# Kernel optimization log

Measured on AMD Instinct MI355X. Metric: run time of the kernel, lower is better.

Reference implementation:

```python
import jax, jax.numpy as jnp
import numpy as np

FEATURE_DIM = 128
NUM_EDGES = 640000
NUM_NODES = 40000


def setup_inputs() -> dict:
    key = jax.random.key(0)
    ks = jax.random.split(key, 10)
    d = FEATURE_DIM
    scale = 1.0 / np.sqrt(d)
    inp = {
        "messages": jax.random.normal(ks[0], (NUM_EDGES, d), dtype=jnp.float32),
        "receivers": jax.random.randint(ks[1], (NUM_EDGES,), 0, NUM_NODES, dtype=jnp.int32),
        "num_segments": NUM_NODES,
        "Wk": jax.random.normal(ks[2], (d, d), dtype=jnp.float32) * scale,
        "bk": jnp.zeros((d,), dtype=jnp.float32),
        "Wv": jax.random.normal(ks[3], (d, d), dtype=jnp.float32) * scale,
        "bv": jnp.zeros((d,), dtype=jnp.float32),
        "Wq": jax.random.normal(ks[4], (d, d), dtype=jnp.float32) * scale,
        "bq": jnp.zeros((d,), dtype=jnp.float32),
        "Wo": jax.random.normal(ks[5], (d, d), dtype=jnp.float32) * scale,
        "bo": jnp.zeros((d,), dtype=jnp.float32),
    }
    return inp


def reference(messages, receivers, num_segments, Wk, bk, Wv, bv, Wq, bq, Wo, bo):
    d = messages.shape[-1]
    # per-edge key/value projections
    keys = messages @ Wk + bk            # [E, d]
    values = messages @ Wv + bv          # [E, d]
    # node-level summed messages -> queries
    summed = jax.ops.segment_sum(messages, receivers, num_segments)  # [N, d]
    queries = summed @ Wq + bq                                       # [N, d]
    # scalar attention score per edge (dot over full feature dim)
    msg_q = queries[receivers]                                       # [E, d]
    scores = jnp.sum(msg_q * keys, axis=-1) / jnp.sqrt(jnp.float32(d))  # [E]
    # segment softmax over edges sharing a receiver
    max_s = jax.ops.segment_max(scores, receivers, num_segments)     # [N]
    exp_s = jnp.exp(scores - max_s[receivers])                       # [E]
    sum_e = jax.ops.segment_sum(exp_s, receivers, num_segments)      # [N]
    attn = exp_s / (sum_e[receivers] + 1e-08)                        # [E]
    # weighted scatter-sum of values, then output projection
    agg = jax.ops.segment_sum(values * attn[:, None], receivers, num_segments)  # [N, d]
    return agg @ Wo + bo
```

## Files before the change

### kernel.cpp

```cpp
#include <hip/hip_runtime.h>

#define D 128
#define RSQRT_D 0.088388347648318440550f
#define NEG_HUGE -3.4e38f
#define NPB 8
#define CAP 288
#define DTHR 20.0f

#define FMA4(acc, s, b) { acc.x += (s)*(b).x; acc.y += (s)*(b).y; acc.z += (s)*(b).z; acc.w += (s)*(b).w; }
#define ADD4(acc, b) { acc.x += (b).x; acc.y += (b).y; acc.z += (b).z; acc.w += (b).w; }
#define MRG4(a) { a.x += __shfl_xor(a.x,32); a.y += __shfl_xor(a.y,32); a.z += __shfl_xor(a.z,32); a.w += __shfl_xor(a.w,32); }
#define SCL4(a, f) { a.x *= (f); a.y *= (f); a.z *= (f); a.w *= (f); }
#define Z4 make_float4(0.f,0.f,0.f,0.f)

#define MERGE_HALVES(mi, si, ci) { \
    float mo_ = __shfl_xor(mi, 32); \
    float so_ = __shfl_xor(si, 32); \
    float4 co_; co_.x = __shfl_xor(ci.x, 32); co_.y = __shfl_xor(ci.y, 32); \
    co_.z = __shfl_xor(ci.z, 32); co_.w = __shfl_xor(ci.w, 32); \
    float mt_ = fmaxf(mi, mo_); \
    float e0_ = __expf(mi - mt_), e1_ = __expf(mo_ - mt_); \
    si = si * e0_ + so_ * e1_; \
    ci.x = ci.x * e0_ + co_.x * e1_; ci.y = ci.y * e0_ + co_.y * e1_; \
    ci.z = ci.z * e0_ + co_.z * e1_; ci.w = ci.w * e0_ + co_.w * e1_; \
}

__global__ __launch_bounds__(256) void prep_kernel(
    const float* __restrict__ Wq, const float* __restrict__ Wk,
    const float* __restrict__ bq, const float* __restrict__ bk,
    const float* __restrict__ Wv, const float* __restrict__ Wo,
    const float* __restrict__ bv,
    float* __restrict__ Wqk, float* __restrict__ bqk,
    float* __restrict__ wqb, float* __restrict__ bqb,
    float* __restrict__ Wvo, float* __restrict__ bvo,
    int* __restrict__ zbase, int zcount) {
    int bid = blockIdx.x, t = threadIdx.x;
    if (bid < 64) {
        int i = bid * 2 + (t >> 7), j = t & 127;
        float a1 = 0.f, a2 = 0.f;
        for (int u = 0; u < D; ++u) {
            a1 += Wq[i * D + u] * Wk[j * D + u];
            a2 += Wv[i * D + u] * Wo[u * D + j];
        }
        Wqk[i * D + j] = a1;
        Wvo[i * D + j] = a2;
    } else if (bid == 64) {
        if (t < D) {
            int j = t;
            float a1 = 0.f, a2 = 0.f, a3 = 0.f;
            for (int u = 0; u < D; ++u) {
                a1 += bq[u] * Wk[j * D + u];
                a2 += Wq[j * D + u] * bk[u];
                a3 += bv[u] * Wo[u * D + j];
            }
            bqk[j] = a1; wqb[j] = a2; bvo[j] = a3;
            if (j == 0) {
                float b = 0.f;
                for (int u = 0; u < D; ++u) b += bq[u] * bk[u];
                *bqb = b;
            }
        }
    } else {
        int idx = (bid - 65) * 256 + t;
        if (idx < zcount) zbase[idx] = 0;
    }
}

__global__ void hist_kernel(const int* __restrict__ recv, int* __restrict__ cnt, int E) {
    int i = blockIdx.x * blockDim.x + threadIdx.x;
    int base = i << 2;
    if (base + 3 < E) {
        int4 r = *(const int4*)(recv + base);
        atomicAdd(&cnt[r.x], 1);
        atomicAdd(&cnt[r.y], 1);
        atomicAdd(&cnt[r.z], 1);
        atomicAdd(&cnt[r.w], 1);
    } else {
        for (int u = base; u < E; ++u) atomicAdd(&cnt[recv[u]], 1);
    }
}

__global__ __launch_bounds__(1024) void scan_kernel(const int* __restrict__ cnt,
                                                    int* __restrict__ start, int N) {
    __shared__ int wsum[16];
    __shared__ int chunk_total;
    int t = threadIdx.x;
    int w = t >> 6, lane = t & 63;
    int running = 0;
    const int4* cnt4 = (const int4*)cnt;
    int nIter = (N + 4095) >> 12;
    int4 v = make_int4(0, 0, 0, 0);
    {
        int i = t << 2;
        if (i < N) v = cnt4[i >> 2];
    }
    for (int it = 0; it < nIter; ++it) {
        int4 vn = make_int4(0, 0, 0, 0);
        {
            int i = ((it + 1) << 12) + (t << 2);
            if (it + 1 < nIter && i < N) vn = cnt4[i >> 2];
        }
        int s0 = v.x, s1 = s0 + v.y, s2 = s1 + v.z, s3 = s2 + v.w;
        int x = s3;
#pragma unroll
        for (int off = 1; off < 64; off <<= 1) {
            int y = __shfl_up(x, off);
            if (lane >= off) x += y;
        }
        if (lane == 63) wsum[w] = x;
        __syncthreads();
        if (w == 0 && lane < 16) {
            int s = wsum[lane];
#pragma unroll
            for (int off = 1; off < 16; off <<= 1) {
                int y = __shfl_up(s, off);
                if (lane >= off) s += y;
            }
            wsum[lane] = s;
            if (lane == 15) chunk_total = s;
        }
        __syncthreads();
        int waveoff = (w == 0) ? 0 : wsum[w - 1];
        int tb = running + waveoff + (x - s3);
        int i = (it << 12) + (t << 2);
        if (i < N) ((int4*)start)[i >> 2] = make_int4(tb, tb + s0, tb + s1, tb + s2);
        running += chunk_total;
        __syncthreads();
        v = vn;
    }
    if (t == 0) start[N] = running;
}

__global__ void fill_kernel(const int* __restrict__ recv, const int* __restrict__ start,
                            int* __restrict__ cursor, int* __restrict__ eidx, int E) {
    int e = blockIdx.x * blockDim.x + threadIdx.x;
    if (e >= E) return;
    int r = recv[e];
    int p = atomicAdd(&cursor[r], 1);
    eidx[start[r] + p] = e;
}

__device__ __forceinline__ float hdot32(float4 f, float4 q) {
    float p = f.x * q.x + f.y * q.y + f.z * q.z + f.w * q.w;
    p += __shfl_xor(p, 1); p += __shfl_xor(p, 2); p += __shfl_xor(p, 4);
    p += __shfl_xor(p, 8); p += __shfl_xor(p, 16);
    return p;
}

#define P1STEP(u, Fx) { \
    int r = j + h + 2 * (u); \
    float4 g_ = Fx; \
    float mk_ = (r < b4) ? 1.f : 0.f; \
    g_.x *= mk_; g_.y *= mk_; g_.z *= mk_; g_.w *= mk_; \
    if (r < b1)      { ADD4(a0, g_); } \
    else if (r < b2) { ADD4(a1, g_); } \
    else if (r < b3) { ADD4(a2, g_); } \
    else             { ADD4(a3, g_); } \
}

#define P3STEP(u, Fx) { \
    int r = j + h + 2 * (u); \
    bool valid_ = r < b4; \
    float4 f_ = Fx; \
    float4 qv_ = (r < b1) ? q0 : (r < b2) ? q1 : (r < b3) ? q2 : q3; \
    float qbv_ = (r < b1) ? qb0 : (r < b2) ? qb1 : (r < b3) ? qb2 : qb3; \
    float sc_ = (hdot32(f_, qv_) + qbv_) * RSQRT_D; \
    float msel_ = (r < b1) ? m0 : (r < b2) ? m1 : (r < b3) ? m2 : m3; \
    if (valid_ && sc_ > msel_ + DTHR) { \
        float fac_ = __expf(msel_ - sc_); \
        if (r < b1)      { sm0 *= fac_; SCL4(c0, fac_); m0 = sc_; } \
        else if (r < b2) { sm1 *= fac_; SCL4(c1, fac_); m1 = sc_; } \
        else if (r < b3) { sm2 *= fac_; SCL4(c2, fac_); m2 = sc_; } \
        else             { sm3 *= fac_; SCL4(c3, fac_); m3 = sc_; } \
        msel_ = sc_; \
    } \
    float wgt_ = valid_ ? __expf(sc_ - msel_) : 0.f; \
    if (r < b1)      { sm0 += wgt_; FMA4(c0, wgt_, f_); } \
    else if (r < b2) { sm1 += wgt_; FMA4(c1, wgt_, f_); } \
    else if (r < b3) { sm2 += wgt_; FMA4(c2, wgt_, f_); } \
    else             { sm3 += wgt_; FMA4(c3, wgt_, f_); } \
}

__global__ __launch_bounds__(128, 3) void mega_kernel(
    const float* __restrict__ msg, const int* __restrict__ eidx,
    const int* __restrict__ start,
    const float* __restrict__ Wqk, const float* __restrict__ bqk,
    const float* __restrict__ wqb, const float* __restrict__ bqbp,
    const float* __restrict__ Wvo, const float* __restrict__ bvo,
    const float* __restrict__ bo,
    float* __restrict__ out, int N) {
    __shared__ float4 sums4[NPB * 32];
    __shared__ float4 qks4[NPB * 32];
    __shared__ int eidx_s[CAP];
    __shared__ float sat[NPB];

    int t = threadIdx.x;
    int lane = t & 63, w = t >> 6;
    int h = lane >> 5;
    int k = lane & 31;
    int base = blockIdx.x * NPB;
    const float4* msg4 = (const float4*)msg;

    int nendB = min(base + NPB, N);
    int s0B = start[base];
    int cntB = start[nendB] - s0B;
    int cc = min(cntB, CAP);
    for (int i = t; i < cc; i += 128) eidx_s[i] = eidx[s0B + i];

    int n0 = base + w * 4;
    int b0 = start[min(n0 + 0, N)] - s0B;
    int b1 = start[min(n0 + 1, N)] - s0B;
    int b2 = start[min(n0 + 2, N)] - s0B;
    int b3 = start[min(n0 + 3, N)] - s0B;
    int b4 = start[min(n0 + 4, N)] - s0B;

    __syncthreads();

    auto loadrow = [&](int r) -> float4 {
        int rI = min(r, b4 - 1);
        int e = (rI < CAP) ? eidx_s[rI] : eidx[s0B + rI];
        return msg4[(size_t)e * 32 + k];
    };

    float4 a0 = Z4, a1 = Z4, a2 = Z4, a3 = Z4;
    if (b0 < b4) {
        int j = b0;
        float4 F0 = loadrow(j + h),      F1 = loadrow(j + h + 2),
               F2 = loadrow(j + h + 4),  F3 = loadrow(j + h + 6),
               F4 = loadrow(j + h + 8),  F5 = loadrow(j + h + 10),
               F6 = loadrow(j + h + 12), F7 = loadrow(j + h + 14);
        for (;;) {
            int jn = j + 16;
            bool more = jn < b4;
            float4 G0, G1, G2, G3, G4, G5, G6, G7;
            if (more) {
                G0 = loadrow(jn + h);      G1 = loadrow(jn + h + 2);
                G2 = loadrow(jn + h + 4);  G3 = loadrow(jn + h + 6);
                G4 = loadrow(jn + h + 8);  G5 = loadrow(jn + h + 10);
                G6 = loadrow(jn + h + 12); G7 = loadrow(jn + h + 14);
            }
            P1STEP(0, F0); P1STEP(1, F1); P1STEP(2, F2); P1STEP(3, F3);
            P1STEP(4, F4); P1STEP(5, F5); P1STEP(6, F6); P1STEP(7, F7);
            if (!more) break;
            F0 = G0; F1 = G1; F2 = G2; F3 = G3;
            F4 = G4; F5 = G5; F6 = G6; F7 = G7;
            j = jn;
        }
    }
    MRG4(a0); MRG4(a1); MRG4(a2); MRG4(a3);
    if (lane < 32) {
        sums4[(w * 4 + 0) * 32 + k] = a0;
        sums4[(w * 4 + 1) * 32 + k] = a1;
        sums4[(w * 4 + 2) * 32 + k] = a2;
        sums4[(w * 4 + 3) * 32 + k] = a3;
    }
    __syncthreads();

    {
        int c = t & 31, slot = t >> 5;
        const float4* B4 = (const float4*)Wqk;
        float4 acc0 = ((const float4*)bqk)[c];
        float4 acc1 = acc0;
        for (int i = 0; i < D; i += 4) {
            float4 aA = sums4[slot * 32 + (i >> 2)];
            float4 aB = sums4[(slot + 4) * 32 + (i >> 2)];
            float4 c0 = B4[(i + 0) * 32 + c];
            float4 c1 = B4[(i + 1) * 32 + c];
            float4 c2 = B4[(i + 2) * 32 + c];
            float4 c3 = B4[(i + 3) * 32 + c];
            FMA4(acc0, aA.x, c0); FMA4(acc0, aA.y, c1); FMA4(acc0, aA.z, c2); FMA4(acc0, aA.w, c3);
            FMA4(acc1, aB.x, c0); FMA4(acc1, aB.y, c1); FMA4(acc1, aB.z, c2); FMA4(acc1, aB.w, c3);
        }
        qks4[slot * 32 + c] = acc0;
        qks4[(slot + 4) * 32 + c] = acc1;
    }
    __syncthreads();

    {
        float4 wv = ((const float4*)wqb)[k];
        float bqb = bqbp[0];
        float4 sv0 = sums4[(w * 4 + 0) * 32 + k];
        float4 sv1 = sums4[(w * 4 + 1) * 32 + k];
        float4 sv2 = sums4[(w * 4 + 2) * 32 + k];
        float4 sv3 = sums4[(w * 4 + 3) * 32 + k];
        float qb0 = hdot32(sv0, wv) + bqb;
        float qb1 = hdot32(sv1, wv) + bqb;
        float qb2 = hdot32(sv2, wv) + bqb;
        float qb3 = hdot32(sv3, wv) + bqb;
        float4 q0 = qks4[(w * 4 + 0) * 32 + k];
        float4 q1 = qks4[(w * 4 + 1) * 32 + k];
        float4 q2 = qks4[(w * 4 + 2) * 32 + k];
        float4 q3 = qks4[(w * 4 + 3) * 32 + k];

        float m0 = NEG_HUGE, m1 = NEG_HUGE, m2 = NEG_HUGE, m3 = NEG_HUGE;
        float sm0 = 0.f, sm1 = 0.f, sm2 = 0.f, sm3 = 0.f;
        float4 c0 = Z4, c1 = Z4, c2 = Z4, c3 = Z4;
        if (b0 < b4) {
            int j = b0;
            float4 F0 = loadrow(j + h),      F1 = loadrow(j + h + 2),
                   F2 = loadrow(j + h + 4),  F3 = loadrow(j + h + 6),
                   F4 = loadrow(j + h + 8),  F5 = loadrow(j + h + 10),
                   F6 = loadrow(j + h + 12), F7 = loadrow(j + h + 14);
            for (;;) {
                int jn = j + 16;
                bool more = jn < b4;
                float4 G0, G1, G2, G3, G4, G5, G6, G7;
                if (more) {
                    G0 = loadrow(jn + h);      G1 = loadrow(jn + h + 2);
                    G2 = loadrow(jn + h + 4);  G3 = loadrow(jn + h + 6);
                    G4 = loadrow(jn + h + 8);  G5 = loadrow(jn + h + 10);
                    G6 = loadrow(jn + h + 12); G7 = loadrow(jn + h + 14);
                }
                P3STEP(0, F0); P3STEP(1, F1); P3STEP(2, F2); P3STEP(3, F3);
                P3STEP(4, F4); P3STEP(5, F5); P3STEP(6, F6); P3STEP(7, F7);
                if (!more) break;
                F0 = G0; F1 = G1; F2 = G2; F3 = G3;
                F4 = G4; F5 = G5; F6 = G6; F7 = G7;
                j = jn;
            }
        }
        MERGE_HALVES(m0, sm0, c0);
        MERGE_HALVES(m1, sm1, c1);
        MERGE_HALVES(m2, sm2, c2);
        MERGE_HALVES(m3, sm3, c3);
        float inv0 = 1.f / (sm0 + 1e-8f);
        float inv1 = 1.f / (sm1 + 1e-8f);
        float inv2 = 1.f / (sm2 + 1e-8f);
        float inv3 = 1.f / (sm3 + 1e-8f);
        if (lane < 32) {
            sums4[(w * 4 + 0) * 32 + k] = make_float4(c0.x * inv0, c0.y * inv0, c0.z * inv0, c0.w * inv0);
            sums4[(w * 4 + 1) * 32 + k] = make_float4(c1.x * inv1, c1.y * inv1, c1.z * inv1, c1.w * inv1);
            sums4[(w * 4 + 2) * 32 + k] = make_float4(c2.x * inv2, c2.y * inv2, c2.z * inv2, c2.w * inv2);
            sums4[(w * 4 + 3) * 32 + k] = make_float4(c3.x * inv3, c3.y * inv3, c3.z * inv3, c3.w * inv3);
        }
        if (lane == 0) {
            sat[w * 4 + 0] = sm0 * inv0;
            sat[w * 4 + 1] = sm1 * inv1;
            sat[w * 4 + 2] = sm2 * inv2;
            sat[w * 4 + 3] = sm3 * inv3;
        }
    }
    __syncthreads();

    {
        int c = t & 31, slot = t >> 5;
        const float4* B4 = (const float4*)Wvo;
        float4 bo4 = ((const float4*)bo)[c];
        float4 bv4 = ((const float4*)bvo)[c];
        float sa0 = sat[slot], sa1 = sat[slot + 4];
        float4 acc0 = make_float4(bo4.x + sa0 * bv4.x, bo4.y + sa0 * bv4.y,
                                  bo4.z + sa0 * bv4.z, bo4.w + sa0 * bv4.w);
        float4 acc1 = make_float4(bo4.x + sa1 * bv4.x, bo4.y + sa1 * bv4.y,
                                  bo4.z + sa1 * bv4.z, bo4.w + sa1 * bv4.w);
        for (int i = 0; i < D; i += 4) {
            float4 aA = sums4[slot * 32 + (i >> 2)];
            float4 aB = sums4[(slot + 4) * 32 + (i >> 2)];
            float4 d0 = B4[(i + 0) * 32 + c];
            float4 d1 = B4[(i + 1) * 32 + c];
            float4 d2 = B4[(i + 2) * 32 + c];
            float4 d3 = B4[(i + 3) * 32 + c];
            FMA4(acc0, aA.x, d0); FMA4(acc0, aA.y, d1); FMA4(acc0, aA.z, d2); FMA4(acc0, aA.w, d3);
            FMA4(acc1, aB.x, d0); FMA4(acc1, aB.y, d1); FMA4(acc1, aB.z, d2); FMA4(acc1, aB.w, d3);
        }
        int nA = base + slot, nB = base + slot + 4;
        if (nA < N) ((float4*)(out + (size_t)nA * D))[c] = acc0;
        if (nB < N) ((float4*)(out + (size_t)nB * D))[c] = acc1;
    }
}


extern "C" void kernel_launch(void* const* d_in, const int* in_sizes, int n_in,
                              void* d_out, int out_size, void* d_ws, size_t ws_size,
                              hipStream_t stream) {
    const float* msg = (const float*)d_in[0];
    const int* recv = (const int*)d_in[1];
    const float* Wk = (const float*)d_in[3];
    const float* bk = (const float*)d_in[4];
    const float* Wv = (const float*)d_in[5];
    const float* bv = (const float*)d_in[6];
    const float* Wq = (const float*)d_in[7];
    const float* bq = (const float*)d_in[8];
    const float* Wo = (const float*)d_in[9];
    const float* bo = (const float*)d_in[10];
    float* out = (float*)d_out;

    int E = in_sizes[0] / D;
    int N = out_size / D;

    char* wsb = (char*)d_ws;
    size_t o = 0;
    auto alloc = [&](size_t elems) {
        void* p = wsb + o;
        o += (elems * 4 + 63) & ~(size_t)63;
        return p;
    };

    int* cnt    = (int*)alloc(2 * (size_t)N);
    int* cursor = cnt + N;
    int* start  = (int*)alloc(N + 1);
    int* eidx   = (int*)alloc(E);
    float* Wqk  = (float*)alloc(D * D);
    float* bqk  = (float*)alloc(D);
    float* wqb  = (float*)alloc(D);
    float* bqb  = (float*)alloc(1);
    float* Wvo  = (float*)alloc(D * D);
    float* bvo  = (float*)alloc(D);

    int zcount = 2 * N;
    int zblocks = (zcount + 255) / 256;
    prep_kernel<<<65 + zblocks, 256, 0, stream>>>(Wq, Wk, bq, bk, Wv, Wo, bv,
                                                  Wqk, bqk, wqb, bqb, Wvo, bvo,
                                                  cnt, zcount);
    int E4 = (E + 3) / 4;
    int nbE4 = (E4 + 255) / 256;
    hist_kernel<<<nbE4, 256, 0, stream>>>(recv, cnt, E);
    scan_kernel<<<1, 1024, 0, stream>>>(cnt, start, N);
    int nbE = (E + 255) / 256;
    fill_kernel<<<nbE, 256, 0, stream>>>(recv, start, cursor, eidx, E);
    mega_kernel<<<(N + NPB - 1) / NPB, 128, 0, stream>>>(msg, eidx, start, Wqk, bqk, wqb, bqb,
                                                         Wvo, bvo, bo, out, N);
}
```

Before: 708.8 us.

## Write gathered message rows to a receiver-sorted buffer for contiguous second pass

During the first segment-sum pass, each gathered message row is also written to a workspace buffer ordered by receiver. The second, softmax-weighted pass then reads that buffer contiguously instead of gathering through the edge index again. This replaces a random gather with a streaming write plus a streaming read, which adds about one extra full-size write and read of the messages. The prefetch depth is halved from 16 to 8 rows and the occupancy hint is raised from 3 to 4 blocks, presumably to cut register pressure. The path only runs when the workspace can hold E*D floats.

```diff
diff --git a/kernel.cpp b/kernel.cpp
--- a/kernel.cpp
+++ b/kernel.cpp
@@ -150,6 +150,7 @@
 #define P1STEP(u, Fx) { \
     int r = j + h + 2 * (u); \
     float4 g_ = Fx; \
+    if (PERM && r < b4) perm4w[(size_t)(s0B + r) * 32 + k] = g_; \
     float mk_ = (r < b4) ? 1.f : 0.f; \
     g_.x *= mk_; g_.y *= mk_; g_.z *= mk_; g_.w *= mk_; \
     if (r < b1)      { ADD4(a0, g_); } \
@@ -181,9 +182,10 @@
     else             { sm3 += wgt_; FMA4(c3, wgt_, f_); } \
 }
 
-__global__ __launch_bounds__(128, 3) void mega_kernel(
+template<int PERM>
+__global__ __launch_bounds__(128, 4) void mega_kernel(
     const float* __restrict__ msg, const int* __restrict__ eidx,
-    const int* __restrict__ start,
+    const int* __restrict__ start, float* __restrict__ perm,
     const float* __restrict__ Wqk, const float* __restrict__ bqk,
     const float* __restrict__ wqb, const float* __restrict__ bqbp,
     const float* __restrict__ Wvo, const float* __restrict__ bvo,
@@ -200,6 +202,8 @@
     int k = lane & 31;
     int base = blockIdx.x * NPB;
     const float4* msg4 = (const float4*)msg;
+    float4* perm4w = (float4*)perm;
+    const float4* perm4c = (const float4*)perm;
 
     int nendB = min(base + NPB, N);
     int s0B = start[base];
@@ -221,29 +225,28 @@
         int e = (rI < CAP) ? eidx_s[rI] : eidx[s0B + rI];
         return msg4[(size_t)e * 32 + k];
     };
+    auto loadrowP = [&](int r) -> float4 {
+        int rI = min(r, b4 - 1);
+        if (PERM) return perm4c[(size_t)(s0B + rI) * 32 + k];
+        else      return loadrow(rI);
+    };
 
     float4 a0 = Z4, a1 = Z4, a2 = Z4, a3 = Z4;
     if (b0 < b4) {
         int j = b0;
-        float4 F0 = loadrow(j + h),      F1 = loadrow(j + h + 2),
-               F2 = loadrow(j + h + 4),  F3 = loadrow(j + h + 6),
-               F4 = loadrow(j + h + 8),  F5 = loadrow(j + h + 10),
-               F6 = loadrow(j + h + 12), F7 = loadrow(j + h + 14);
+        float4 F0 = loadrow(j + h), F1 = loadrow(j + h + 2),
+               F2 = loadrow(j + h + 4), F3 = loadrow(j + h + 6);
         for (;;) {
-            int jn = j + 16;
+            int jn = j + 8;
             bool more = jn < b4;
-            float4 G0, G1, G2, G3, G4, G5, G6, G7;
+            float4 G0, G1, G2, G3;
             if (more) {
-                G0 = loadrow(jn + h);      G1 = loadrow(jn + h + 2);
-                G2 = loadrow(jn + h + 4);  G3 = loadrow(jn + h + 6);
-                G4 = loadrow(jn + h + 8);  G5 = loadrow(jn + h + 10);
-                G6 = loadrow(jn + h + 12); G7 = loadrow(jn + h + 14);
+                G0 = loadrow(jn + h); G1 = loadrow(jn + h + 2);
+                G2 = loadrow(jn + h + 4); G3 = loadrow(jn + h + 6);
             }
             P1STEP(0, F0); P1STEP(1, F1); P1STEP(2, F2); P1STEP(3, F3);
-            P1STEP(4, F4); P1STEP(5, F5); P1STEP(6, F6); P1STEP(7, F7);
             if (!more) break;
             F0 = G0; F1 = G1; F2 = G2; F3 = G3;
-            F4 = G4; F5 = G5; F6 = G6; F7 = G7;
             j = jn;
         }
     }
@@ -297,25 +300,19 @@
         float4 c0 = Z4, c1 = Z4, c2 = Z4, c3 = Z4;
         if (b0 < b4) {
             int j = b0;
-            float4 F0 = loadrow(j + h),      F1 = loadrow(j + h + 2),
-                   F2 = loadrow(j + h + 4),  F3 = loadrow(j + h + 6),
-                   F4 = loadrow(j + h + 8),  F5 = loadrow(j + h + 10),
-                   F6 = loadrow(j + h + 12), F7 = loadrow(j + h + 14);
+            float4 F0 = loadrowP(j + h), F1 = loadrowP(j + h + 2),
+                   F2 = loadrowP(j + h + 4), F3 = loadrowP(j + h + 6);
             for (;;) {
-                int jn = j + 16;
+                int jn = j + 8;
                 bool more = jn < b4;
-                float4 G0, G1, G2, G3, G4, G5, G6, G7;
+                float4 G0, G1, G2, G3;
                 if (more) {
-                    G0 = loadrow(jn + h);      G1 = loadrow(jn + h + 2);
-                    G2 = loadrow(jn + h + 4);  G3 = loadrow(jn + h + 6);
-                    G4 = loadrow(jn + h + 8);  G5 = loadrow(jn + h + 10);
-                    G6 = loadrow(jn + h + 12); G7 = loadrow(jn + h + 14);
+                    G0 = loadrowP(jn + h); G1 = loadrowP(jn + h + 2);
+                    G2 = loadrowP(jn + h + 4); G3 = loadrowP(jn + h + 6);
                 }
                 P3STEP(0, F0); P3STEP(1, F1); P3STEP(2, F2); P3STEP(3, F3);
-                P3STEP(4, F4); P3STEP(5, F5); P3STEP(6, F6); P3STEP(7, F7);
                 if (!more) break;
                 F0 = G0; F1 = G1; F2 = G2; F3 = G3;
-                F4 = G4; F5 = G5; F6 = G6; F7 = G7;
                 j = jn;
             }
         }
@@ -405,6 +402,8 @@
     float* bqb  = (float*)alloc(1);
     float* Wvo  = (float*)alloc(D * D);
     float* bvo  = (float*)alloc(D);
+    float* perm = (float*)(wsb + o);
+    bool use_perm = (o + (size_t)E * D * 4) <= ws_size;
 
     int zcount = 2 * N;
     int zblocks = (zcount + 255) / 256;
@@ -417,6 +416,12 @@
     scan_kernel<<<1, 1024, 0, stream>>>(cnt, start, N);
     int nbE = (E + 255) / 256;
     fill_kernel<<<nbE, 256, 0, stream>>>(recv, start, cursor, eidx, E);
-    mega_kernel<<<(N + NPB - 1) / NPB, 128, 0, stream>>>(msg, eidx, start, Wqk, bqk, wqb, bqb,
-                                                         Wvo, bvo, bo, out, N);
-}
+    int nblk = (N + NPB - 1) / NPB;
+    if (use_perm) {
+        mega_kernel<1><<<nblk, 128, 0, stream>>>(msg, eidx, start, perm, Wqk, bqk, wqb, bqb,
+                                                 Wvo, bvo, bo, out, N);
+    } else {
+        mega_kernel<0><<<nblk, 128, 0, stream>>>(msg, eidx, start, nullptr, Wqk, bqk, wqb, bqb,
+                                                 Wvo, bvo, bo, out, N);
+    }
+}
```

Result: no change. 712.5 us (+0.5%).

## Keep first 48 edge rows in registers across both passes to avoid reloading

Applied to the files above, without the earlier changes.

The first 48 gathered message rows of each warp's node group (about 6 per node at an average degree of 16 per node... per 4 nodes) are loaded once into 24 float4 registers and reused in both the segment-sum pass and the attention pass. Remaining edges fall back to a smaller 4-row software-pipelined loop. This aims to cut the second gather of message rows from memory, at the cost of much higher register pressure, which under launch_bounds(128,3) may cause spills or lower occupancy. The tail loop also has less memory-level parallelism than the previous 16-row prefetch.

```diff
diff --git a/kernel.cpp b/kernel.cpp
--- a/kernel.cpp
+++ b/kernel.cpp
@@ -181,6 +181,9 @@
     else             { sm3 += wgt_; FMA4(c3, wgt_, f_); } \
 }
 
+#define P1G(jo, Ra, Rb, Rc, Rd) { int j = b0 + (jo); P1STEP(0, Ra); P1STEP(1, Rb); P1STEP(2, Rc); P1STEP(3, Rd); }
+#define P3G(jo, Ra, Rb, Rc, Rd) { int j = b0 + (jo); P3STEP(0, Ra); P3STEP(1, Rb); P3STEP(2, Rc); P3STEP(3, Rd); }
+
 __global__ __launch_bounds__(128, 3) void mega_kernel(
     const float* __restrict__ msg, const int* __restrict__ eidx,
     const int* __restrict__ start,
@@ -222,29 +225,39 @@
         return msg4[(size_t)e * 32 + k];
     };
 
+    float4 R00 = Z4, R01 = Z4, R02 = Z4, R03 = Z4,
+           R10 = Z4, R11 = Z4, R12 = Z4, R13 = Z4,
+           R20 = Z4, R21 = Z4, R22 = Z4, R23 = Z4,
+           R30 = Z4, R31 = Z4, R32 = Z4, R33 = Z4,
+           R40 = Z4, R41 = Z4, R42 = Z4, R43 = Z4,
+           R50 = Z4, R51 = Z4, R52 = Z4, R53 = Z4;
+
     float4 a0 = Z4, a1 = Z4, a2 = Z4, a3 = Z4;
     if (b0 < b4) {
-        int j = b0;
-        float4 F0 = loadrow(j + h),      F1 = loadrow(j + h + 2),
-               F2 = loadrow(j + h + 4),  F3 = loadrow(j + h + 6),
-               F4 = loadrow(j + h + 8),  F5 = loadrow(j + h + 10),
-               F6 = loadrow(j + h + 12), F7 = loadrow(j + h + 14);
-        for (;;) {
-            int jn = j + 16;
-            bool more = jn < b4;
-            float4 G0, G1, G2, G3, G4, G5, G6, G7;
-            if (more) {
-                G0 = loadrow(jn + h);      G1 = loadrow(jn + h + 2);
-                G2 = loadrow(jn + h + 4);  G3 = loadrow(jn + h + 6);
-                G4 = loadrow(jn + h + 8);  G5 = loadrow(jn + h + 10);
-                G6 = loadrow(jn + h + 12); G7 = loadrow(jn + h + 14);
+        R00 = loadrow(b0 + h +  0); R01 = loadrow(b0 + h +  2); R02 = loadrow(b0 + h +  4); R03 = loadrow(b0 + h +  6);
+        R10 = loadrow(b0 + h +  8); R11 = loadrow(b0 + h + 10); R12 = loadrow(b0 + h + 12); R13 = loadrow(b0 + h + 14);
+        R20 = loadrow(b0 + h + 16); R21 = loadrow(b0 + h + 18); R22 = loadrow(b0 + h + 20); R23 = loadrow(b0 + h + 22);
+        R30 = loadrow(b0 + h + 24); R31 = loadrow(b0 + h + 26); R32 = loadrow(b0 + h + 28); R33 = loadrow(b0 + h + 30);
+        R40 = loadrow(b0 + h + 32); R41 = loadrow(b0 + h + 34); R42 = loadrow(b0 + h + 36); R43 = loadrow(b0 + h + 38);
+        R50 = loadrow(b0 + h + 40); R51 = loadrow(b0 + h + 42); R52 = loadrow(b0 + h + 44); R53 = loadrow(b0 + h + 46);
+        P1G( 0, R00, R01, R02, R03);
+        P1G( 8, R10, R11, R12, R13);
+        P1G(16, R20, R21, R22, R23);
+        P1G(24, R30, R31, R32, R33);
+        P1G(32, R40, R41, R42, R43);
+        P1G(40, R50, R51, R52, R53);
+        int j = b0 + 48;
+        if (j < b4) {
+            float4 F0 = loadrow(j + h), F1 = loadrow(j + h + 2);
+            for (;;) {
+                int jn = j + 4;
+                bool more = jn < b4;
+                float4 G0, G1;
+                if (more) { G0 = loadrow(jn + h); G1 = loadrow(jn + h + 2); }
+                P1STEP(0, F0); P1STEP(1, F1);
+                if (!more) break;
+                F0 = G0; F1 = G1; j = jn;
             }
-            P1STEP(0, F0); P1STEP(1, F1); P1STEP(2, F2); P1STEP(3, F3);
-            P1STEP(4, F4); P1STEP(5, F5); P1STEP(6, F6); P1STEP(7, F7);
-            if (!more) break;
-            F0 = G0; F1 = G1; F2 = G2; F3 = G3;
-            F4 = G4; F5 = G5; F6 = G6; F7 = G7;
-            j = jn;
         }
     }
     MRG4(a0); MRG4(a1); MRG4(a2); MRG4(a3);
@@ -264,12 +277,12 @@
         for (int i = 0; i < D; i += 4) {
             float4 aA = sums4[slot * 32 + (i >> 2)];
             float4 aB = sums4[(slot + 4) * 32 + (i >> 2)];
-            float4 c0 = B4[(i + 0) * 32 + c];
-            float4 c1 = B4[(i + 1) * 32 + c];
-            float4 c2 = B4[(i + 2) * 32 + c];
-            float4 c3 = B4[(i + 3) * 32 + c];
-            FMA4(acc0, aA.x, c0); FMA4(acc0, aA.y, c1); FMA4(acc0, aA.z, c2); FMA4(acc0, aA.w, c3);
-            FMA4(acc1, aB.x, c0); FMA4(acc1, aB.y, c1); FMA4(acc1, aB.z, c2); FMA4(acc1, aB.w, c3);
+            float4 w0 = B4[(i + 0) * 32 + c];
+            float4 w1 = B4[(i + 1) * 32 + c];
+            float4 w2 = B4[(i + 2) * 32 + c];
+            float4 w3 = B4[(i + 3) * 32 + c];
+            FMA4(acc0, aA.x, w0); FMA4(acc0, aA.y, w1); FMA4(acc0, aA.z, w2); FMA4(acc0, aA.w, w3);
+            FMA4(acc1, aB.x, w0); FMA4(acc1, aB.y, w1); FMA4(acc1, aB.z, w2); FMA4(acc1, aB.w, w3);
         }
         qks4[slot * 32 + c] = acc0;
         qks4[(slot + 4) * 32 + c] = acc1;
@@ -296,27 +309,24 @@
         float sm0 = 0.f, sm1 = 0.f, sm2 = 0.f, sm3 = 0.f;
         float4 c0 = Z4, c1 = Z4, c2 = Z4, c3 = Z4;
         if (b0 < b4) {
-            int j = b0;
-            float4 F0 = loadrow(j + h),      F1 = loadrow(j + h + 2),
-                   F2 = loadrow(j + h + 4),  F3 = loadrow(j + h + 6),
-                   F4 = loadrow(j + h + 8),  F5 = loadrow(j + h + 10),
-                   F6 = loadrow(j + h + 12), F7 = loadrow(j + h + 14);
-            for (;;) {
-                int jn = j + 16;
-                bool more = jn < b4;
-                float4 G0, G1, G2, G3, G4, G5, G6, G7;
-                if (more) {
-                    G0 = loadrow(jn + h);      G1 = loadrow(jn + h + 2);
-                    G2 = loadrow(jn + h + 4);  G3 = loadrow(jn + h + 6);
-                    G4 = loadrow(jn + h + 8);  G5 = loadrow(jn + h + 10);
-                    G6 = loadrow(jn + h + 12); G7 = loadrow(jn + h + 14);
+            P3G( 0, R00, R01, R02, R03);
+            P3G( 8, R10, R11, R12, R13);
+            P3G(16, R20, R21, R22, R23);
+            P3G(24, R30, R31, R32, R33);
+            P3G(32, R40, R41, R42, R43);
+            P3G(40, R50, R51, R52, R53);
+            int j = b0 + 48;
+            if (j < b4) {
+                float4 F0 = loadrow(j + h), F1 = loadrow(j + h + 2);
+                for (;;) {
+                    int jn = j + 4;
+                    bool more = jn < b4;
+                    float4 G0, G1;
+                    if (more) { G0 = loadrow(jn + h); G1 = loadrow(jn + h + 2); }
+                    P3STEP(0, F0); P3STEP(1, F1);
+                    if (!more) break;
+                    F0 = G0; F1 = G1; j = jn;
                 }
-                P3STEP(0, F0); P3STEP(1, F1); P3STEP(2, F2); P3STEP(3, F3);
-                P3STEP(4, F4); P3STEP(5, F5); P3STEP(6, F6); P3STEP(7, F7);
-                if (!more) break;
-                F0 = G0; F1 = G1; F2 = G2; F3 = G3;
-                F4 = G4; F5 = G5; F6 = G6; F7 = G7;
-                j = jn;
             }
         }
         MERGE_HALVES(m0, sm0, c0);
```

Measured after the change: 680.7 us. 4.0% less time.
